# Performance work log

Measured on AMD Instinct MI355X. Metric: run time of the kernel, lower is better.

Reference implementation:

```python
import jax, jax.numpy as jnp
import numpy as np
from jax import lax

B, H, W = 2, 720, 1280
EPS = 1e-7


def setup_inputs() -> dict:
    key = jax.random.key(0)
    k0, k1, k2, k3, k4, k5 = jax.random.split(key, 6)
    return {
        "img0": jax.random.uniform(k0, (B, 3, H, W), jnp.float32),
        "img1": jax.random.uniform(k1, (B, 3, H, W), jnp.float32),
        "flow0": jax.random.normal(k2, (B, 2, H, W), jnp.float32),
        "flow1": jax.random.normal(k3, (B, 2, H, W), jnp.float32),
        "z0": jax.random.normal(k4, (B, 1, H, W), jnp.float32),
        "z1": jax.random.normal(k5, (B, 1, H, W), jnp.float32),
        "k": 5,
    }


def _softsplat(inp, flow):
    """Forward (splatting) warp. inp [B,C,H,W]; flow [B,2,H,W], ch0 = x-disp, ch1 = y-disp."""
    Bn, C, Hn, Wn = inp.shape
    gx = jnp.arange(Wn, dtype=inp.dtype)
    gy = jnp.arange(Hn, dtype=inp.dtype)
    fx = gx[None, None, :] + flow[:, 0]  # [B,H,W] target x
    fy = gy[None, :, None] + flow[:, 1]  # [B,H,W] target y
    x0 = jnp.floor(fx); x1 = x0 + 1.0
    y0 = jnp.floor(fy); y1 = y0 + 1.0
    # 4 bilinear corners: (x0,y0) (x1,y0) (x0,y1) (x1,y1)
    xs = jnp.stack([x0, x1, x0, x1])            # [4,B,H,W]
    ys = jnp.stack([y0, y0, y1, y1])
    wts = jnp.stack([(x1 - fx) * (y1 - fy),
                     (fx - x0) * (y1 - fy),
                     (x1 - fx) * (fy - y0),
                     (fx - x0) * (fy - y0)])    # [4,B,H,W]
    xi = xs.astype(jnp.int32)
    yi = ys.astype(jnp.int32)
    valid = (xi >= 0) & (xi < Wn) & (yi >= 0) & (yi < Hn)
    wts = jnp.where(valid, wts, 0.0)
    idx = jnp.clip(yi, 0, Hn - 1) * Wn + jnp.clip(xi, 0, Wn - 1)  # [4,B,H,W]
    idx = jnp.moveaxis(idx, 1, 0).reshape(Bn, 4 * Hn * Wn)
    wts = jnp.moveaxis(wts, 1, 0)                                 # [B,4,H,W]

    def splat_one(inp_b, idx_b, w_b):
        # inp_b [C,H,W], idx_b [4HW], w_b [4,H,W]
        vals = (inp_b[None] * w_b[:, None]).transpose(1, 0, 2, 3).reshape(C, 4 * Hn * Wn)
        out = jnp.zeros((C, Hn * Wn), inp_b.dtype)
        out = out.at[:, idx_b].add(vals)
        return out.reshape(C, Hn, Wn)

    return jax.vmap(splat_one)(inp, idx, wts)


def _forewarp_soft(img, flow, metric):
    """flow_forewarp(img, flow, mode='sm', metric=metric, mask=True)."""
    flow = flow[:, ::-1]  # .flip(dims=(1,)) in the original
    Bn, _, Hn, Wn = img.shape
    ones = jnp.ones((Bn, 1, Hn, Wn), img.dtype)
    img_m = jnp.concatenate([img, ones], axis=1)          # mask channel appended
    w = jnp.exp(metric)                                   # softmax-splat weight
    inp = jnp.concatenate([img_m * w, w], axis=1)         # [B, C+2, H, W]
    out = _softsplat(inp, flow)
    return out[:, :-1] / (out[:, -1:] + EPS)              # normalize by splatted weight


def _morph_open(x, k):
    # kornia.morphology.opening with a flat k x k ones SE = min-pool then max-pool
    if k == 0:
        return x
    win = (1, 1, k, k)
    one = (1, 1, 1, 1)
    er = lax.reduce_window(x, jnp.inf, lax.min, win, one, "SAME")
    return lax.reduce_window(er, -jnp.inf, lax.max, win, one, "SAME")


def reference(img0, img1, flow0, flow1, z0, z1, k):
    t = 0.5
    flow0_ = (1.0 - t) * flow0
    flow1_ = t * flow1
    f01 = _forewarp_soft(img0, flow1_, z1)
    f10 = _forewarp_soft(img1, flow0_, z0)
    f01i, f01m = f01[:, :-1], lax.stop_gradient(_morph_open(f01[:, -1:], k))
    f10i, f10m = f10[:, :-1], lax.stop_gradient(_morph_open(f10[:, -1:], k))
    base0 = f01m * f01i + (1.0 - f01m) * f10i
    base1 = f10m * f10i + (1.0 - f10m) * f01i
    # flat concat of ans = [[base0, base1, f01i, f10i], [flow0_, flow1_], [f01m, f10m]] -> 18 ch
    return jnp.concatenate([base0, base1, f01i, f10i, flow0_, flow1_, f01m, f10m], axis=1)
```

## Files before the change

### kernel.cpp

```cpp
#include <hip/hip_runtime.h>
#include <math.h>

#define Hh 720
#define Ww 1280
#define Bb 2
#define HW (Hh*Ww)
#define OUTC 18
#define EPSF 1e-7f

#define DMAX 2.0f
#define OWN_W 32
#define OWN_H 8
#define SRC_W (OWN_W + 5)
#define SRC_H (OWN_H + 5)
#define NSRC (SRC_W * SRC_H)
#define TILES_X (Ww / OWN_W)
#define TILES_Y (Hh / OWN_H)
#define NTILES (Bb * TILES_X * TILES_Y)

__global__ __launch_bounds__(256) void far_prepass_kernel(
    const float* __restrict__ img0, const float* __restrict__ img1,
    const float* __restrict__ flow0, const float* __restrict__ flow1,
    const float* __restrict__ z0, const float* __restrict__ z1,
    float* __restrict__ out, int* __restrict__ flags)
{
    int i = blockIdx.x * 256 + threadIdx.x;
    if (i >= Bb * HW) return;
    int b = i / HW;
    int p = i - b * HW;
    int y = p / Ww;
    int x = p - y * Ww;

    float f1x = flow1[((size_t)b * 2 + 1) * HW + p];
    float f1y = flow1[((size_t)b * 2 + 0) * HW + p];
    float f0x = flow0[((size_t)b * 2 + 1) * HW + p];
    float f0y = flow0[((size_t)b * 2 + 0) * HW + p];
    float dxs[2] = { 0.5f * f1x, 0.5f * f0x };
    float dys[2] = { 0.5f * f1y, 0.5f * f0y };

    out[((size_t)b * OUTC + 14) * HW + p] = 0.5f * f1y;
    out[((size_t)b * OUTC + 15) * HW + p] = 0.5f * f1x;

    for (int d = 0; d < 2; ++d) {
        float dx = dxs[d], dy = dys[d];
        if (fabsf(dx) <= DMAX && fabsf(dy) <= DMAX) continue;

        const float* img = d ? img1 : img0;
        const float* met = d ? z0 : z1;
        float fx = (float)x + dx;
        float fy = (float)y + dy;
        float w  = expf(met[(size_t)b * HW + p]);
        float v0 = img[((size_t)b * 3 + 0) * HW + p] * w;
        float v1 = img[((size_t)b * 3 + 1) * HW + p] * w;
        float v2 = img[((size_t)b * 3 + 2) * HW + p] * w;

        float x0f = floorf(fx), y0f = floorf(fy);
        float x1f = x0f + 1.0f, y1f = y0f + 1.0f;
        int   x0  = (int)x0f,  y0i = (int)y0f;
        float wxs[2] = { x1f - fx, fx - x0f };
        float wys[2] = { y1f - fy, fy - y0f };

        float* accImg = out + ((size_t)b * OUTC + (d ? 9 : 6)) * HW;
        float* accW   = out + ((size_t)b * OUTC + (d ? 17 : 16)) * HW;

        for (int cy = 0; cy < 2; ++cy) {
            int yy = y0i + cy;
            if (yy < 0 || yy >= Hh) continue;
            for (int cx = 0; cx < 2; ++cx) {
                int xx = x0 + cx;
                if (xx < 0 || xx >= Ww) continue;
                float wt = wxs[cx] * wys[cy];
                if (wt == 0.0f) continue;
                int q = yy * Ww + xx;
                atomicAdd(accImg + q,          v0 * wt);
                atomicAdd(accImg + HW + q,     v1 * wt);
                atomicAdd(accImg + 2 * HW + q, v2 * wt);
                atomicAdd(accW + q,            w  * wt);
                if (flags)
                    flags[(b * TILES_Y + yy / OWN_H) * TILES_X + xx / OWN_W] = 1;
            }
        }
    }
}

__global__ __launch_bounds__(256) void gather_splat_kernel(
    const float* __restrict__ img0, const float* __restrict__ img1,
    const float* __restrict__ flow0, const float* __restrict__ flow1,
    const float* __restrict__ z0, const float* __restrict__ z1,
    float* __restrict__ out, const int* __restrict__ flags)
{
    __shared__ float4 geo[2][SRC_H][SRC_W];
    __shared__ float4 vw [2][SRC_H][SRC_W];

    int wg   = blockIdx.x;
    int wgid = (wg & 7) * (NTILES / 8) + (wg >> 3);
    int b    = wgid / (TILES_X * TILES_Y);
    int rr   = wgid - b * (TILES_X * TILES_Y);
    int tY   = rr / TILES_X;
    int tX   = rr - tY * TILES_X;
    const int tX0 = tX * OWN_W;
    const int tY0 = tY * OWN_H;

    for (int c = threadIdx.x; c < NSRC; c += 256) {
        int cy = c / SRC_W, cx = c - cy * SRC_W;
        int sx = tX0 + cx - 2;
        int sy = tY0 + cy - 2;
        bool inimg = (sx >= 0) && (sx < Ww) && (sy >= 0) && (sy < Hh);
        int p = min(max(sy, 0), Hh - 1) * Ww + min(max(sx, 0), Ww - 1);

        float f1x = flow1[((size_t)b * 2 + 1) * HW + p];
        float f1y = flow1[((size_t)b * 2 + 0) * HW + p];
        float f0x = flow0[((size_t)b * 2 + 1) * HW + p];
        float f0y = flow0[((size_t)b * 2 + 0) * HW + p];
        float zz1 = z1[(size_t)b * HW + p];
        float zz0 = z0[(size_t)b * HW + p];
        float a0 = img0[((size_t)b * 3 + 0) * HW + p];
        float a1 = img0[((size_t)b * 3 + 1) * HW + p];
        float a2 = img0[((size_t)b * 3 + 2) * HW + p];
        float c0 = img1[((size_t)b * 3 + 0) * HW + p];
        float c1 = img1[((size_t)b * 3 + 1) * HW + p];
        float c2 = img1[((size_t)b * 3 + 2) * HW + p];

        float dx0 = 0.5f * f1x, dy0 = 0.5f * f1y;
        float dx1 = 0.5f * f0x, dy1 = 0.5f * f0y;
        bool l0 = inimg && (fabsf(dx0) <= DMAX) && (fabsf(dy0) <= DMAX);
        bool l1 = inimg && (fabsf(dx1) <= DMAX) && (fabsf(dy1) <= DMAX);
        float w0 = l0 ? expf(zz1) : 0.0f;
        float w1 = l1 ? expf(zz0) : 0.0f;

        float fx0 = (float)sx + dx0, fy0 = (float)sy + dy0;
        float fx1 = (float)sx + dx1, fy1 = (float)sy + dy1;
        float x0f0 = floorf(fx0), y0f0 = floorf(fy0);
        float x0f1 = floorf(fx1), y0f1 = floorf(fy1);

        geo[0][cy][cx] = make_float4(l0 ? x0f0 - (float)sx : 1e9f,
                                     l0 ? y0f0 - (float)sy : 1e9f,
                                     fx0 - x0f0, fy0 - y0f0);
        geo[1][cy][cx] = make_float4(l1 ? x0f1 - (float)sx : 1e9f,
                                     l1 ? y0f1 - (float)sy : 1e9f,
                                     fx1 - x0f1, fy1 - y0f1);
        vw[0][cy][cx] = make_float4(a0 * w0, a1 * w0, a2 * w0, w0);
        vw[1][cy][cx] = make_float4(c0 * w1, c1 * w1, c2 * w1, w1);
    }
    __syncthreads();

    const int qlx = threadIdx.x & (OWN_W - 1);
    const int qly = threadIdx.x >> 5;

    float acc[2][4];
#pragma unroll
    for (int d = 0; d < 2; ++d)
#pragma unroll
        for (int c = 0; c < 4; ++c) acc[d][c] = 0.0f;

#pragma unroll
    for (int d = 0; d < 2; ++d) {
#pragma unroll
        for (int oy = 0; oy < 6; ++oy) {
            const float oyf = (float)(oy - 2);
#pragma unroll
            for (int ox = 0; ox < 6; ++ox) {
                const float oxf = (float)(ox - 2);
                float4 g = geo[d][qly + oy][qlx + ox];
                float tx = g.x + oxf;
                float ty = g.y + oyf;
                float wx = (tx == 0.0f) ? (1.0f - g.z) : ((tx == -1.0f) ? g.z : 0.0f);
                float wy = (ty == 0.0f) ? (1.0f - g.w) : ((ty == -1.0f) ? g.w : 0.0f);
                float wt = wx * wy;
                if (wt > 0.0f) {
                    float4 v = vw[d][qly + oy][qlx + ox];
                    acc[d][0] += wt * v.x;
                    acc[d][1] += wt * v.y;
                    acc[d][2] += wt * v.z;
                    acc[d][3] += wt * v.w;
                }
            }
        }
    }

    const size_t q = (size_t)(tY0 + qly) * Ww + (tX0 + qlx);
    bool flagged = true;
    if (flags)
        flagged = flags[(b * TILES_Y + tY) * TILES_X + tX] != 0;

#pragma unroll
    for (int d = 0; d < 2; ++d) {
        float* accImg = out + ((size_t)b * OUTC + (d ? 9 : 6)) * HW;
        float* accW   = out + ((size_t)b * OUTC + (d ? 17 : 16)) * HW;
        float s0 = acc[d][0];
        float s1 = acc[d][1];
        float s2 = acc[d][2];
        float sw = acc[d][3];
        if (flagged) {
            s0 += accImg[q];
            s1 += accImg[HW + q];
            s2 += accImg[2 * HW + q];
            sw += accW[q];
        }
        float inv = 1.0f / (sw + EPSF);
        accImg[q]          = s0 * inv;
        accImg[HW + q]     = s1 * inv;
        accImg[2 * HW + q] = s2 * inv;
        accW[q]            = sw;
    }
}

__global__ __launch_bounds__(256) void erode_kernel(float* __restrict__ out,
                                                    const int* __restrict__ kptr)
{
    int i = blockIdx.x * 256 + threadIdx.x;
    if (i >= Bb * HW) return;
    int b = i / HW;
    int p = i - b * HW;
    int y = p / Ww;
    int x = p - y * Ww;
    int k = *kptr;

    const float* s01 = out + ((size_t)b * OUTC + 16) * HW;
    const float* s10 = out + ((size_t)b * OUTC + 17) * HW;
    float* er01 = out + ((size_t)b * OUTC + 12) * HW;
    float* er10 = out + ((size_t)b * OUTC + 13) * HW;

    if (k <= 0) { er01[p] = s01[p]; er10[p] = s10[p]; return; }

    float m0 = INFINITY, m1 = INFINITY;
    if (k == 5) {
#pragma unroll
        for (int dy = -2; dy <= 2; ++dy) {
            int yy = min(max(y + dy, 0), Hh - 1);
#pragma unroll
            for (int dx = -2; dx <= 2; ++dx) {
                int xx = min(max(x + dx, 0), Ww - 1);
                int q = yy * Ww + xx;
                m0 = fminf(m0, s01[q]);
                m1 = fminf(m1, s10[q]);
            }
        }
    } else {
        int lo = (k - 1) / 2, hi = (k - 1) - lo;
        for (int dy = -lo; dy <= hi; ++dy) {
            int yy = y + dy;
            if (yy < 0 || yy >= Hh) continue;
            for (int dx = -lo; dx <= hi; ++dx) {
                int xx = x + dx;
                if (xx < 0 || xx >= Ww) continue;
                int q = yy * Ww + xx;
                m0 = fminf(m0, s01[q]);
                m1 = fminf(m1, s10[q]);
            }
        }
    }
    er01[p] = m0;
    er10[p] = m1;
}

__global__ __launch_bounds__(256) void fuse_kernel(float* __restrict__ out,
                                                   const int* __restrict__ kptr)
{
    int i = blockIdx.x * 256 + threadIdx.x;
    if (i >= Bb * HW) return;
    int b = i / HW;
    int p = i - b * HW;
    int y = p / Ww;
    int x = p - y * Ww;
    int k = *kptr;

    const float* er01 = out + ((size_t)b * OUTC + 12) * HW;
    const float* er10 = out + ((size_t)b * OUTC + 13) * HW;

    float o0, o1;
    if (k <= 0) {
        o0 = er01[p];
        o1 = er10[p];
    } else if (k == 5) {
        o0 = -INFINITY; o1 = -INFINITY;
#pragma unroll
        for (int dy = -2; dy <= 2; ++dy) {
            int yy = min(max(y + dy, 0), Hh - 1);
#pragma unroll
            for (int dx = -2; dx <= 2; ++dx) {
                int xx = min(max(x + dx, 0), Ww - 1);
                int q = yy * Ww + xx;
                o0 = fmaxf(o0, er01[q]);
                o1 = fmaxf(o1, er10[q]);
            }
        }
    } else {
        int lo = (k - 1) / 2, hi = (k - 1) - lo;
        o0 = -INFINITY; o1 = -INFINITY;
        for (int dy = -lo; dy <= hi; ++dy) {
            int yy = y + dy;
            if (yy < 0 || yy >= Hh) continue;
            for (int dx = -lo; dx <= hi; ++dx) {
                int xx = x + dx;
                if (xx < 0 || xx >= Ww) continue;
                int q = yy * Ww + xx;
                o0 = fmaxf(o0, er01[q]);
                o1 = fmaxf(o1, er10[q]);
            }
        }
    }

    float m01 = o0 / (o0 + EPSF);
    float m10 = o1 / (o1 + EPSF);

    float* ob = out + (size_t)b * OUTC * HW;
#pragma unroll
    for (int c = 0; c < 3; ++c) {
        float f01i = ob[((size_t)6 + c) * HW + p];
        float f10i = ob[((size_t)9 + c) * HW + p];
        ob[((size_t)0 + c) * HW + p] = m01 * f01i + (1.0f - m01) * f10i;
        ob[((size_t)3 + c) * HW + p] = m10 * f10i + (1.0f - m10) * f01i;
    }
    ob[(size_t)16 * HW + p] = m01;
    ob[(size_t)17 * HW + p] = m10;
}

__global__ __launch_bounds__(256) void flow_kernel(const float* __restrict__ flow0,
                                                   float* __restrict__ out)
{
    int i = blockIdx.x * 256 + threadIdx.x;
    if (i >= Bb * 2 * HW) return;
    int b = i / (2 * HW);
    int r = i - b * 2 * HW;
    int c = r / HW;
    int p = r - c * HW;
    out[((size_t)b * OUTC + 12 + c) * HW + p] = 0.5f * flow0[((size_t)b * 2 + c) * HW + p];
}

extern "C" void kernel_launch(void* const* d_in, const int* in_sizes, int n_in,
                              void* d_out, int out_size, void* d_ws, size_t ws_size,
                              hipStream_t stream) {
    const float* img0  = (const float*)d_in[0];
    const float* img1  = (const float*)d_in[1];
    const float* flow0 = (const float*)d_in[2];
    const float* flow1 = (const float*)d_in[3];
    const float* z0    = (const float*)d_in[4];
    const float* z1    = (const float*)d_in[5];
    const int*   kptr  = (const int*)d_in[6];
    float* out = (float*)d_out;

    for (int b = 0; b < Bb; ++b) {
        hipMemsetAsync(out + ((size_t)b * OUTC + 6) * HW, 0, (size_t)6 * HW * sizeof(float), stream);
        hipMemsetAsync(out + ((size_t)b * OUTC + 16) * HW, 0, (size_t)2 * HW * sizeof(float), stream);
    }

    int* flags = nullptr;
    if (d_ws && ws_size >= (size_t)NTILES * sizeof(int)) {
        flags = (int*)d_ws;
        hipMemsetAsync(flags, 0, (size_t)NTILES * sizeof(int), stream);
    }

    int n = Bb * HW;
    int blocks = (n + 255) / 256;

    far_prepass_kernel<<<blocks, 256, 0, stream>>>(img0, img1, flow0, flow1, z0, z1, out, flags);
    gather_splat_kernel<<<NTILES, 256, 0, stream>>>(img0, img1, flow0, flow1, z0, z1, out, flags);
    erode_kernel<<<blocks, 256, 0, stream>>>(out, kptr);
    fuse_kernel<<<blocks, 256, 0, stream>>>(out, kptr);
    int n2 = Bb * 2 * HW;
    flow_kernel<<<(n2 + 255) / 256, 256, 0, stream>>>(flow0, out);
}
```

Before: 315.8 us.

## Tile erode/dilate through LDS with separable min/max and halve splat LDS

Adds tiled erode5 and fuse5 kernels for k<=5. Each loads a haloed tile into shared memory and applies the k×k min/max as a row pass followed by a column pass, which replaces 25 global reads per pixel. The old per-pixel kernels now return early unless k>5, and both variants are launched every call. The gather splat kernel now processes the two warp directions one after another through a single shared buffer, halving its LDS footprint to allow more occupancy, at the cost of an extra barrier.

```diff
diff --git a/kernel.cpp b/kernel.cpp
--- a/kernel.cpp
+++ b/kernel.cpp
@@ -17,6 +17,9 @@
 #define TILES_X (Ww / OWN_W)
 #define TILES_Y (Hh / OWN_H)
 #define NTILES (Bb * TILES_X * TILES_Y)
+
+#define EW (OWN_W + 4)
+#define EH (OWN_H + 4)
 
 __global__ __launch_bounds__(256) void far_prepass_kernel(
     const float* __restrict__ img0, const float* __restrict__ img1,
@@ -89,8 +92,8 @@
     const float* __restrict__ z0, const float* __restrict__ z1,
     float* __restrict__ out, const int* __restrict__ flags)
 {
-    __shared__ float4 geo[2][SRC_H][SRC_W];
-    __shared__ float4 vw [2][SRC_H][SRC_W];
+    __shared__ float4 geo[SRC_H][SRC_W];
+    __shared__ float4 vw [SRC_H][SRC_W];
 
     int wg   = blockIdx.x;
     int wgid = (wg & 7) * (NTILES / 8) + (wg >> 3);
@@ -101,49 +104,6 @@
     const int tX0 = tX * OWN_W;
     const int tY0 = tY * OWN_H;
 
-    for (int c = threadIdx.x; c < NSRC; c += 256) {
-        int cy = c / SRC_W, cx = c - cy * SRC_W;
-        int sx = tX0 + cx - 2;
-        int sy = tY0 + cy - 2;
-        bool inimg = (sx >= 0) && (sx < Ww) && (sy >= 0) && (sy < Hh);
-        int p = min(max(sy, 0), Hh - 1) * Ww + min(max(sx, 0), Ww - 1);
-
-        float f1x = flow1[((size_t)b * 2 + 1) * HW + p];
-        float f1y = flow1[((size_t)b * 2 + 0) * HW + p];
-        float f0x = flow0[((size_t)b * 2 + 1) * HW + p];
-        float f0y = flow0[((size_t)b * 2 + 0) * HW + p];
-        float zz1 = z1[(size_t)b * HW + p];
-        float zz0 = z0[(size_t)b * HW + p];
-        float a0 = img0[((size_t)b * 3 + 0) * HW + p];
-        float a1 = img0[((size_t)b * 3 + 1) * HW + p];
-        float a2 = img0[((size_t)b * 3 + 2) * HW + p];
-        float c0 = img1[((size_t)b * 3 + 0) * HW + p];
-        float c1 = img1[((size_t)b * 3 + 1) * HW + p];
-        float c2 = img1[((size_t)b * 3 + 2) * HW + p];
-
-        float dx0 = 0.5f * f1x, dy0 = 0.5f * f1y;
-        float dx1 = 0.5f * f0x, dy1 = 0.5f * f0y;
-        bool l0 = inimg && (fabsf(dx0) <= DMAX) && (fabsf(dy0) <= DMAX);
-        bool l1 = inimg && (fabsf(dx1) <= DMAX) && (fabsf(dy1) <= DMAX);
-        float w0 = l0 ? expf(zz1) : 0.0f;
-        float w1 = l1 ? expf(zz0) : 0.0f;
-
-        float fx0 = (float)sx + dx0, fy0 = (float)sy + dy0;
-        float fx1 = (float)sx + dx1, fy1 = (float)sy + dy1;
-        float x0f0 = floorf(fx0), y0f0 = floorf(fy0);
-        float x0f1 = floorf(fx1), y0f1 = floorf(fy1);
-
-        geo[0][cy][cx] = make_float4(l0 ? x0f0 - (float)sx : 1e9f,
-                                     l0 ? y0f0 - (float)sy : 1e9f,
-                                     fx0 - x0f0, fy0 - y0f0);
-        geo[1][cy][cx] = make_float4(l1 ? x0f1 - (float)sx : 1e9f,
-                                     l1 ? y0f1 - (float)sy : 1e9f,
-                                     fx1 - x0f1, fy1 - y0f1);
-        vw[0][cy][cx] = make_float4(a0 * w0, a1 * w0, a2 * w0, w0);
-        vw[1][cy][cx] = make_float4(c0 * w1, c1 * w1, c2 * w1, w1);
-    }
-    __syncthreads();
-
     const int qlx = threadIdx.x & (OWN_W - 1);
     const int qly = threadIdx.x >> 5;
 
@@ -155,20 +115,53 @@
 
 #pragma unroll
     for (int d = 0; d < 2; ++d) {
+        if (d) __syncthreads();
+
+        const float* flw = d ? flow0 : flow1;
+        const float* met = d ? z0 : z1;
+        const float* img = d ? img1 : img0;
+
+        for (int c = threadIdx.x; c < NSRC; c += 256) {
+            int cy = c / SRC_W, cx = c - cy * SRC_W;
+            int sx = tX0 + cx - 2;
+            int sy = tY0 + cy - 2;
+            bool inimg = (sx >= 0) && (sx < Ww) && (sy >= 0) && (sy < Hh);
+            int p = min(max(sy, 0), Hh - 1) * Ww + min(max(sx, 0), Ww - 1);
+
+            float fxv = flw[((size_t)b * 2 + 1) * HW + p];
+            float fyv = flw[((size_t)b * 2 + 0) * HW + p];
+            float zz  = met[(size_t)b * HW + p];
+            float i0  = img[((size_t)b * 3 + 0) * HW + p];
+            float i1  = img[((size_t)b * 3 + 1) * HW + p];
+            float i2  = img[((size_t)b * 3 + 2) * HW + p];
+
+            float dx = 0.5f * fxv, dy = 0.5f * fyv;
+            bool l = inimg && (fabsf(dx) <= DMAX) && (fabsf(dy) <= DMAX);
+            float w = l ? expf(zz) : 0.0f;
+
+            float fx = (float)sx + dx, fy = (float)sy + dy;
+            float x0f = floorf(fx), y0f = floorf(fy);
+            geo[cy][cx] = make_float4(l ? x0f - (float)sx : 1e9f,
+                                      l ? y0f - (float)sy : 1e9f,
+                                      fx - x0f, fy - y0f);
+            vw[cy][cx] = make_float4(i0 * w, i1 * w, i2 * w, w);
+        }
+        __syncthreads();
+
 #pragma unroll
         for (int oy = 0; oy < 6; ++oy) {
             const float oyf = (float)(oy - 2);
 #pragma unroll
             for (int ox = 0; ox < 6; ++ox) {
                 const float oxf = (float)(ox - 2);
-                float4 g = geo[d][qly + oy][qlx + ox];
+                float4 g = geo[qly + oy][qlx + ox];
                 float tx = g.x + oxf;
                 float ty = g.y + oyf;
                 float wx = (tx == 0.0f) ? (1.0f - g.z) : ((tx == -1.0f) ? g.z : 0.0f);
                 float wy = (ty == 0.0f) ? (1.0f - g.w) : ((ty == -1.0f) ? g.w : 0.0f);
                 float wt = wx * wy;
                 if (wt > 0.0f) {
-                    float4 v = vw[d][qly + oy][qlx + ox];
+                    float4 v = vw[qly + oy][qlx + ox];
                     acc[d][0] += wt * v.x;
                     acc[d][1] += wt * v.y;
                     acc[d][2] += wt * v.z;
@@ -205,49 +198,176 @@
     }
 }
 
+__global__ __launch_bounds__(256) void erode5_kernel(float* __restrict__ out,
+                                                     const int* __restrict__ kptr)
+{
+    __shared__ float s2  [2][EH][EW];
+    __shared__ float rmin[2][EH][OWN_W];
+
+    int k = *kptr;
+    if (k > 5) return;
+
+    int wg   = blockIdx.x;
+    int wgid = (wg & 7) * (NTILES / 8) + (wg >> 3);
+    int b    = wgid / (TILES_X * TILES_Y);
+    int rr   = wgid - b * (TILES_X * TILES_Y);
+    int tY   = rr / TILES_X;
+    int tX   = rr - tY * TILES_X;
+    const int tX0 = tX * OWN_W;
+    const int tY0 = tY * OWN_H;
+
+    const float* s01 = out + ((size_t)b * OUTC + 16) * HW;
+    const float* s10 = out + ((size_t)b * OUTC + 17) * HW;
+    float* er01 = out + ((size_t)b * OUTC + 12) * HW;
+    float* er10 = out + ((size_t)b * OUTC + 13) * HW;
+
+    const int r  = threadIdx.x >> 5;
+    const int xc = threadIdx.x & 31;
+    const size_t qp = (size_t)(tY0 + r) * Ww + (tX0 + xc);
+
+    if (k <= 0) { er01[qp] = s01[qp]; er10[qp] = s10[qp]; return; }
+
+    const int lo = (k - 1) / 2;
+    const int ew = OWN_W + k - 1;
+    const int eh = OWN_H + k - 1;
+
+    for (int c = threadIdx.x; c < eh * ew; c += 256) {
+        int i = c / ew, j = c - i * ew;
+        int gy = min(max(tY0 - lo + i, 0), Hh - 1);
+        int gx = min(max(tX0 - lo + j, 0), Ww - 1);
+        size_t p = (size_t)gy * Ww + gx;
+        s2[0][i][j] = s01[p];
+        s2[1][i][j] = s10[p];
+    }
+    __syncthreads();
+
+    for (int c = threadIdx.x; c < eh * OWN_W; c += 256) {
+        int i = c / OWN_W, x = c - i * OWN_W;
+        float m0 = s2[0][i][x], m1 = s2[1][i][x];
+        for (int t = 1; t < k; ++t) {
+            m0 = fminf(m0, s2[0][i][x + t]);
+            m1 = fminf(m1, s2[1][i][x + t]);
+        }
+        rmin[0][i][x] = m0;
+        rmin[1][i][x] = m1;
+    }
+    __syncthreads();
+
+    float m0 = rmin[0][r][xc], m1 = rmin[1][r][xc];
+    for (int t = 1; t < k; ++t) {
+        m0 = fminf(m0, rmin[0][r + t][xc]);
+        m1 = fminf(m1, rmin[1][r + t][xc]);
+    }
+    er01[qp] = m0;
+    er10[qp] = m1;
+}
+
+__global__ __launch_bounds__(256) void fuse5_kernel(float* __restrict__ out,
+                                                    const int* __restrict__ kptr)
+{
+    __shared__ float e2  [2][EH][EW];
+    __shared__ float rmax[2][EH][OWN_W];
+
+    int k = *kptr;
+    if (k > 5) return;
+
+    int wg   = blockIdx.x;
+    int wgid = (wg & 7) * (NTILES / 8) + (wg >> 3);
+    int b    = wgid / (TILES_X * TILES_Y);
+    int rr   = wgid - b * (TILES_X * TILES_Y);
+    int tY   = rr / TILES_X;
+    int tX   = rr - tY * TILES_X;
+    const int tX0 = tX * OWN_W;
+    const int tY0 = tY * OWN_H;
+
+    const float* er01 = out + ((size_t)b * OUTC + 12) * HW;
+    const float* er10 = out + ((size_t)b * OUTC + 13) * HW;
+
+    const int r  = threadIdx.x >> 5;
+    const int xc = threadIdx.x & 31;
+    const size_t qp = (size_t)(tY0 + r) * Ww + (tX0 + xc);
+
+    float o0, o1;
+    if (k <= 0) {
+        o0 = er01[qp];
+        o1 = er10[qp];
+    } else {
+        const int lo = (k - 1) / 2;
+        const int ew = OWN_W + k - 1;
+        const int eh = OWN_H + k - 1;
+
+        for (int c = threadIdx.x; c < eh * ew; c += 256) {
+            int i = c / ew, j = c - i * ew;
+            int gy = min(max(tY0 - lo + i, 0), Hh - 1);
+            int gx = min(max(tX0 - lo + j, 0), Ww - 1);
+            size_t p = (size_t)gy * Ww + gx;
+            e2[0][i][j] = er01[p];
+            e2[1][i][j] = er10[p];
+        }
+        __syncthreads();
+
+        for (int c = threadIdx.x; c < eh * OWN_W; c += 256) {
+            int i = c / OWN_W, x = c - i * OWN_W;
+            float m0 = e2[0][i][x], m1 = e2[1][i][x];
+            for (int t = 1; t < k; ++t) {
+                m0 = fmaxf(m0, e2[0][i][x + t]);
+                m1 = fmaxf(m1, e2[1][i][x + t]);
+            }
+            rmax[0][i][x] = m0;
+            rmax[1][i][x] = m1;
+        }
+        __syncthreads();
+
+        o0 = rmax[0][r][xc]; o1 = rmax[1][r][xc];
+        for (int t = 1; t < k; ++t) {
+            o0 = fmaxf(o0, rmax[0][r + t][xc]);
+            o1 = fmaxf(o1, rmax[1][r + t][xc]);
+        }
+    }
+
+    float m01 = o0 / (o0 + EPSF);
+    float m10 = o1 / (o1 + EPSF);
+
+    float* ob = out + (size_t)b * OUTC * HW;
+#pragma unroll
+    for (int c = 0; c < 3; ++c) {
+        float f01i = ob[((size_t)6 + c) * HW + qp];
+        float f10i = ob[((size_t)9 + c) * HW + qp];
+        ob[((size_t)0 + c) * HW + qp] = m01 * f01i + (1.0f - m01) * f10i;
+        ob[((size_t)3 + c) * HW + qp] = m10 * f10i + (1.0f - m10) * f01i;
+    }
+    ob[(size_t)16 * HW + qp] = m01;
+    ob[(size_t)17 * HW + qp] = m10;
+}
+
 __global__ __launch_bounds__(256) void erode_kernel(float* __restrict__ out,
                                                     const int* __restrict__ kptr)
 {
+    int k = *kptr;
+    if (k <= 5) return;
     int i = blockIdx.x * 256 + threadIdx.x;
     if (i >= Bb * HW) return;
     int b = i / HW;
     int p = i - b * HW;
     int y = p / Ww;
     int x = p - y * Ww;
-    int k = *kptr;
 
     const float* s01 = out + ((size_t)b * OUTC + 16) * HW;
     const float* s10 = out + ((size_t)b * OUTC + 17) * HW;
     float* er01 = out + ((size_t)b * OUTC + 12) * HW;
     float* er10 = out + ((size_t)b * OUTC + 13) * HW;
 
-    if (k <= 0) { er01[p] = s01[p]; er10[p] = s10[p]; return; }
-
+    int lo = (k - 1) / 2, hi = (k - 1) - lo;
     float m0 = INFINITY, m1 = INFINITY;
-    if (k == 5) {
-#pragma unroll
-        for (int dy = -2; dy <= 2; ++dy) {
-            int yy = min(max(y + dy, 0), Hh - 1);
-#pragma unroll
-            for (int dx = -2; dx <= 2; ++dx) {
-                int xx = min(max(x + dx, 0), Ww - 1);
-                int q = yy * Ww + xx;
-                m0 = fminf(m0, s01[q]);
-                m1 = fminf(m1, s10[q]);
-            }
-        }
-    } else {
-        int lo = (k - 1) / 2, hi = (k - 1) - lo;
-        for (int dy = -lo; dy <= hi; ++dy) {
-            int yy = y + dy;
-            if (yy < 0 || yy >= Hh) continue;
-            for (int dx = -lo; dx <= hi; ++dx) {
-                int xx = x + dx;
-                if (xx < 0 || xx >= Ww) continue;
-                int q = yy * Ww + xx;
-                m0 = fminf(m0, s01[q]);
-                m1 = fminf(m1, s10[q]);
-            }
+    for (int dy = -lo; dy <= hi; ++dy) {
+        int yy = y + dy;
+        if (yy < 0 || yy >= Hh) continue;
+        for (int dx = -lo; dx <= hi; ++dx) {
+            int xx = x + dx;
+            if (xx < 0 || xx >= Ww) continue;
+            int q = yy * Ww + xx;
+            m0 = fminf(m0, s01[q]);
+            m1 = fminf(m1, s10[q]);
         }
     }
     er01[p] = m0;
@@ -257,47 +377,29 @@
 __global__ __launch_bounds__(256) void fuse_kernel(float* __restrict__ out,
                                                    const int* __restrict__ kptr)
 {
+    int k = *kptr;
+    if (k <= 5) return;
     int i = blockIdx.x * 256 + threadIdx.x;
     if (i >= Bb * HW) return;
     int b = i / HW;
     int p = i - b * HW;
     int y = p / Ww;
     int x = p - y * Ww;
-    int k = *kptr;
 
     const float* er01 = out + ((size_t)b * OUTC + 12) * HW;
     const float* er10 = out + ((size_t)b * OUTC + 13) * HW;
 
-    float o0, o1;
-    if (k <= 0) {
-        o0 = er01[p];
-        o1 = er10[p];
-    } else if (k == 5) {
-        o0 = -INFINITY; o1 = -INFINITY;
-#pragma unroll
-        for (int dy = -2; dy <= 2; ++dy) {
-            int yy = min(max(y + dy, 0), Hh - 1);
-#pragma unroll
-            for (int dx = -2; dx <= 2; ++dx) {
-                int xx = min(max(x + dx, 0), Ww - 1);
-                int q = yy * Ww + xx;
-                o0 = fmaxf(o0, er01[q]);
-                o1 = fmaxf(o1, er10[q]);
-            }
-        }
-    } else {
-        int lo = (k - 1) / 2, hi = (k - 1) - lo;
-        o0 = -INFINITY; o1 = -INFINITY;
-        for (int dy = -lo; dy <= hi; ++dy) {
-            int yy = y + dy;
-            if (yy < 0 || yy >= Hh) continue;
-            for (int dx = -lo; dx <= hi; ++dx) {
-                int xx = x + dx;
-                if (xx < 0 || xx >= Ww) continue;
-                int q = yy * Ww + xx;
-                o0 = fmaxf(o0, er01[q]);
-                o1 = fmaxf(o1, er10[q]);
-            }
+    int lo = (k - 1) / 2, hi = (k - 1) - lo;
+    float o0 = -INFINITY, o1 = -INFINITY;
+    for (int dy = -lo; dy <= hi; ++dy) {
+        int yy = y + dy;
+        if (yy < 0 || yy >= Hh) continue;
+        for (int dx = -lo; dx <= hi; ++dx) {
+            int xx = x + dx;
+            if (xx < 0 || xx >= Ww) continue;
+            int q = yy * Ww + xx;
+            o0 = fmaxf(o0, er01[q]);
+            o1 = fmaxf(o1, er10[q]);
         }
     }
 
@@ -356,7 +458,9 @@
 
     far_prepass_kernel<<<blocks, 256, 0, stream>>>(img0, img1, flow0, flow1, z0, z1, out, flags);
     gather_splat_kernel<<<NTILES, 256, 0, stream>>>(img0, img1, flow0, flow1, z0, z1, out, flags);
+    erode5_kernel<<<NTILES, 256, 0, stream>>>(out, kptr);
     erode_kernel<<<blocks, 256, 0, stream>>>(out, kptr);
+    fuse5_kernel<<<NTILES, 256, 0, stream>>>(out, kptr);
     fuse_kernel<<<blocks, 256, 0, stream>>>(out, kptr);
     int n2 = Bb * 2 * HW;
     flow_kernel<<<(n2 + 255) / 256, 256, 0, stream>>>(flow0, out);
```

Measured after the change: 302.5 us. 4.2% less time.
